# Kernel optimization log

Measured on AMD Instinct MI355X. Metric: run time of the kernel, lower is better.

## Reference

```python
import jax, jax.numpy as jnp
import numpy as np

D_MODEL = 1024
N_HEADS = 16
HEAD = D_MODEL // N_HEADS  # 64
D_FF = 4096
LN_EPS = 1e-5


def _layernorm(x, g, b):
    mu = jnp.mean(x, axis=-1, keepdims=True)
    var = jnp.mean(jnp.square(x - mu), axis=-1, keepdims=True)
    return (x - mu) * jax.lax.rsqrt(var + LN_EPS) * g + b


def _mha(q_in, k_in, v_in, Wq, Wk, Wv, bv, causal):
    # Wq/Wk/Wv: [H, d_model, head]; bv: [H, head] (value proj has bias, q/k do not)
    q = jnp.einsum('bsd,hde->bhse', q_in, Wq)
    k = jnp.einsum('btd,hde->bhte', k_in, Wk)
    v = jnp.einsum('btd,hde->bhte', v_in, Wv) + bv[None, :, None, :]
    scale = HEAD ** -0.5
    scores = jnp.einsum('bhse,bhte->bhst', q, k) * scale
    if causal:
        S, T = scores.shape[-2], scores.shape[-1]
        mask = jnp.tril(jnp.ones((S, T), dtype=bool))
        scores = jnp.where(mask, scores, -jnp.inf)
    p = jax.nn.softmax(scores, axis=-1)
    o = jnp.einsum('bhst,bhte->bhse', p, v)  # [B,H,S,head]
    B, H, S, E = o.shape
    return o.transpose(0, 2, 1, 3).reshape(B, S, H * E)  # concat heads in order


def setup_inputs() -> dict:
    key = jax.random.key(0)
    ks = jax.random.split(key, 20)
    B, S, T = 2, 2048, 2048
    sd = D_MODEL ** -0.5
    inp = {
        'input_tensor': jax.random.normal(ks[0], (B, S, D_MODEL), jnp.float32),
        'encoder_output': jax.random.normal(ks[1], (B, T, D_MODEL), jnp.float32),
        # masked self-attention params
        'Wq1': jax.random.normal(ks[2], (N_HEADS, D_MODEL, HEAD), jnp.float32) * sd,
        'Wk1': jax.random.normal(ks[3], (N_HEADS, D_MODEL, HEAD), jnp.float32) * sd,
        'Wv1': jax.random.normal(ks[4], (N_HEADS, D_MODEL, HEAD), jnp.float32) * sd,
        'bv1': jnp.zeros((N_HEADS, HEAD), jnp.float32),
        # cross-attention params
        'Wq2': jax.random.normal(ks[5], (N_HEADS, D_MODEL, HEAD), jnp.float32) * sd,
        'Wk2': jax.random.normal(ks[6], (N_HEADS, D_MODEL, HEAD), jnp.float32) * sd,
        'Wv2': jax.random.normal(ks[7], (N_HEADS, D_MODEL, HEAD), jnp.float32) * sd,
        'bv2': jnp.zeros((N_HEADS, HEAD), jnp.float32),
        # layernorms
        'g1': jnp.ones((D_MODEL,), jnp.float32), 'be1': jnp.zeros((D_MODEL,), jnp.float32),
        'g2': jnp.ones((D_MODEL,), jnp.float32), 'be2': jnp.zeros((D_MODEL,), jnp.float32),
        'g3': jnp.ones((D_MODEL,), jnp.float32), 'be3': jnp.zeros((D_MODEL,), jnp.float32),
        # FFN
        'Wf1': jax.random.normal(ks[8], (D_MODEL, D_FF), jnp.float32) * sd,
        'bf1': jnp.zeros((D_FF,), jnp.float32),
        'Wf2': jax.random.normal(ks[9], (D_FF, D_MODEL), jnp.float32) * (D_FF ** -0.5),
        'bf2': jnp.zeros((D_MODEL,), jnp.float32),
    }
    return inp


def reference(input_tensor, encoder_output, Wq1, Wk1, Wv1, bv1, Wq2, Wk2, Wv2, bv2,
              g1, be1, g2, be2, g3, be3, Wf1, bf1, Wf2, bf2):
    x = input_tensor
    # masked (causal) self-attention; dropout is identity in eval
    sa = _mha(x, x, x, Wq1, Wk1, Wv1, bv1, causal=True)
    x = _layernorm(sa + input_tensor, g1, be1)
    # cross-attention with encoder output (no mask)
    ca = _mha(x, encoder_output, encoder_output, Wq2, Wk2, Wv2, bv2, causal=False)
    x = _layernorm(x + ca, g2, be2)
    # FFN
    ffn = jax.nn.relu(x @ Wf1 + bf1) @ Wf2 + bf2
    x = _layernorm(x + ffn, g3, be3)
    return x
```

## Files before the change

kernel.cpp:

```cpp
#include <hip/hip_runtime.h>
#include <stdint.h>
#include <stddef.h>

typedef __attribute__((ext_vector_type(8))) short short8;
typedef __attribute__((ext_vector_type(4))) short short4_t;
typedef __attribute__((ext_vector_type(4))) float float4_t;
typedef __attribute__((ext_vector_type(4))) unsigned uint4_t;

#define DEV static __device__ __forceinline__

#define QSCALE 0.18033688011112042f

DEV short f2bf(float f) {
  unsigned u = __builtin_bit_cast(unsigned, f);
  u = (u + 0x7FFFu + ((u >> 16) & 1u)) >> 16;
  return (short)(unsigned short)u;
}

DEV void load_lds16(const short* g, short* l) {
  __builtin_amdgcn_global_load_lds((const __attribute__((address_space(1))) void*)g,
                                   (__attribute__((address_space(3))) void*)l,
                                   16, 0, 0);
}

__global__ __launch_bounds__(256) void transpose_cvt(const float* __restrict__ src,
                                                     short* __restrict__ dst,
                                                     int R, int C) {
  __shared__ float t[64][65];
  src += (size_t)blockIdx.z * R * C;
  dst += (size_t)blockIdx.z * R * C;
  const int tid = threadIdx.x;
  const int r0 = blockIdx.y * 64, c0 = blockIdx.x * 64;
#pragma unroll
  for (int i = 0; i < 16; i++) {
    int r = i * 4 + (tid >> 6);
    t[r][tid & 63] = src[(size_t)(r0 + r) * C + c0 + (tid & 63)];
  }
  __syncthreads();
#pragma unroll
  for (int i = 0; i < 16; i++) {
    int c = i * 4 + (tid >> 6);
    dst[(size_t)(c0 + c) * R + r0 + (tid & 63)] = f2bf(t[tid & 63][c]);
  }
}

__global__ __launch_bounds__(256) void cvt_bf16(const float* __restrict__ in,
                                                short* __restrict__ out, int n4) {
  int i = blockIdx.x * 256 + threadIdx.x;
  if (i < n4) {
    float4_t v = ((const float4_t*)in)[i];
    short4_t o;
    o.x = f2bf(v.x); o.y = f2bf(v.y); o.z = f2bf(v.z); o.w = f2bf(v.w);
    ((short4_t*)out)[i] = o;
  }
}

struct GemmArgs {
  const short* A;
  const short* Bt;
  int M, N, K;
  float* outf;
  short* outb;
  short* Qo;
  short* Ko;
  short* Vt;
  const float* bias;
};

template <int MODE>
DEV void scatter1(const GemmArgs& args, int row, int col, float v) {
  if constexpr (MODE == 0) {
    int sel = col >> 10, cc = col & 1023;
    int h = cc >> 6, e = cc & 63;
    int b_ = row >> 11, s = row & 2047;
    if (sel == 0)
      args.Qo[(((size_t)(b_ * 16 + h)) * 2048 + s) * 64 + e] = f2bf(v * QSCALE);
    else if (sel == 1)
      args.Ko[(((size_t)(b_ * 16 + h)) * 2048 + s) * 64 + e] = f2bf(v);
    else {
      v += args.bias[cc];
      args.Vt[(((size_t)(b_ * 16 + h)) * 64 + e) * 2048 + s] = f2bf(v);
    }
  } else if constexpr (MODE == 1) {
    int h = col >> 6, e = col & 63;
    int b_ = row >> 11, s = row & 2047;
    args.Qo[(((size_t)(b_ * 16 + h)) * 2048 + s) * 64 + e] = f2bf(v * QSCALE);
  } else if constexpr (MODE == 2) {
    int sel = col >> 10, cc = col & 1023;
    int h = cc >> 6, e = cc & 63;
    int b_ = row >> 11, s = row & 2047;
    if (sel == 0)
      args.Ko[(((size_t)(b_ * 16 + h)) * 2048 + s) * 64 + e] = f2bf(v);
    else {
      v += args.bias[cc];
      args.Vt[(((size_t)(b_ * 16 + h)) * 64 + e) * 2048 + s] = f2bf(v);
    }
  } else if constexpr (MODE == 3) {
    v += args.bias[col];
    v = v > 0.f ? v : 0.f;
    args.outb[(size_t)row * args.N + col] = f2bf(v);
  } else {
    v += args.bias[col];
    args.outf[(size_t)row * args.N + col] = v;
  }
}

template <int MODE>
__global__ __launch_bounds__(256) void gemm_k(GemmArgs args) {
  constexpr int BM = 128, BK = 64;
  __shared__ short As[2][BM * BK];
  __shared__ short Bs[2][BM * BK];
  const int tid = threadIdx.x;
  const int lane = tid & 63;
  const int w = tid >> 6;
  const int wr = w >> 1, wc = w & 1;

  const int nwgx = gridDim.x;
  const int nwg = nwgx * gridDim.y;
  const int orig = blockIdx.y * nwgx + blockIdx.x;
  const int q8 = nwg >> 3;
  const int swz = (orig & 7) * q8 + (orig >> 3);
  const int row0 = (swz / nwgx) * BM;
  const int col0 = (swz % nwgx) * BM;

  const int K = args.K;
  const short* Ab = args.A + (size_t)row0 * K;
  const short* Bb = args.Bt + (size_t)col0 * K;
  float4_t acc[4][4] = {};
  const int r = lane & 15, kg = lane >> 4, rx = r & 7;

  auto stage = [&](int buf, int k0) {
#pragma unroll
    for (int i = 0; i < 4; i++) {
      int c = i * 256 + tid;
      int rw = c >> 3, sc = (c & 7) ^ (rw & 7);
      load_lds16(Ab + (size_t)rw * K + k0 + sc * 8, &As[buf][c * 8]);
    }
#pragma unroll
    for (int i = 0; i < 4; i++) {
      int c = i * 256 + tid;
      int rw = c >> 3, sc = (c & 7) ^ (rw & 7);
      load_lds16(Bb + (size_t)rw * K + k0 + sc * 8, &Bs[buf][c * 8]);
    }
  };

  stage(0, 0);
  __syncthreads();
  int buf = 0;
  const int nk = K / BK;
  for (int t = 0; t < nk; t++) {
    if (t + 1 < nk) stage(buf ^ 1, (t + 1) * BK);
#pragma unroll
    for (int kk = 0; kk < BK; kk += 32) {
      const int ch = kk >> 3;
      short8 a[4], b[4];
#pragma unroll
      for (int m = 0; m < 4; m++)
        a[m] = *(const short8*)&As[buf][(wr * 64 + m * 16 + r) * BK + ((ch + kg) ^ rx) * 8];
#pragma unroll
      for (int n = 0; n < 4; n++)
        b[n] = *(const short8*)&Bs[buf][(wc * 64 + n * 16 + r) * BK + ((ch + kg) ^ rx) * 8];
#pragma unroll
      for (int m = 0; m < 4; m++)
#pragma unroll
        for (int n = 0; n < 4; n++)
          acc[m][n] = __builtin_amdgcn_mfma_f32_16x16x32_bf16(a[m], b[n], acc[m][n], 0, 0, 0);
    }
    __syncthreads();
    buf ^= 1;
  }

#pragma unroll
  for (int m = 0; m < 4; m++)
#pragma unroll
    for (int n = 0; n < 4; n++)
#pragma unroll
      for (int j = 0; j < 4; j++)
        scatter1<MODE>(args, row0 + wr * 64 + m * 16 + kg * 4 + j,
                       col0 + wc * 64 + n * 16 + r, acc[m][n][j]);
}

template <int MODE>
__global__ __launch_bounds__(512, 2) void gemm256_k(GemmArgs args) {
  extern __shared__ short lds[];
  const int tid = threadIdx.x;
  const int lane = tid & 63;
  const int w = tid >> 6;
  const int wr = w >> 2, wc = w & 3;

  const int nwgx = gridDim.x;
  const int nwg = nwgx * gridDim.y;
  const int orig = blockIdx.y * nwgx + blockIdx.x;
  const int q8 = nwg >> 3;
  const int swz = (orig & 7) * q8 + (orig >> 3);
  const int row0 = (swz / nwgx) * 256;
  const int col0 = (swz % nwgx) * 256;

  const int K = args.K;
  const short* Ab = args.A + (size_t)row0 * K;
  const short* Bb = args.Bt + (size_t)col0 * K;
  const int r = lane & 15, kg = lane >> 4, rx = r & 7;
  float4_t acc[8][4] = {};

  auto stage = [&](int buf, int k0) {
    short* Ad = lds + buf * 16384;
    short* Bd = lds + 32768 + buf * 16384;
#pragma unroll
    for (int i = 0; i < 4; i++) {
      int c = i * 512 + tid;
      int rw = c >> 3, sc = (c & 7) ^ (rw & 7);
      load_lds16(Ab + (size_t)rw * K + k0 + sc * 8, Ad + c * 8);
    }
#pragma unroll
    for (int i = 0; i < 4; i++) {
      int c = i * 512 + tid;
      int rw = c >> 3, sc = (c & 7) ^ (rw & 7);
      load_lds16(Bb + (size_t)rw * K + k0 + sc * 8, Bd + c * 8);
    }
  };

  stage(0, 0);
  __syncthreads();
  int buf = 0;
  const int nk = K / 64;
  for (int t = 0; t < nk; t++) {
    if (t + 1 < nk) stage(buf ^ 1, (t + 1) * 64);
    const short* Ar = lds + buf * 16384;
    const short* Br = lds + 32768 + buf * 16384;
#pragma unroll
    for (int kk = 0; kk < 64; kk += 32) {
      const int ch = kk >> 3;
      short8 a[8], b[4];
#pragma unroll
      for (int m = 0; m < 8; m++)
        a[m] = *(const short8*)&Ar[(wr * 128 + m * 16 + r) * 64 + ((ch + kg) ^ rx) * 8];
#pragma unroll
      for (int n = 0; n < 4; n++)
        b[n] = *(const short8*)&Br[(wc * 64 + n * 16 + r) * 64 + ((ch + kg) ^ rx) * 8];
#pragma unroll
      for (int m = 0; m < 8; m++)
#pragma unroll
        for (int n = 0; n < 4; n++)
          acc[m][n] = __builtin_amdgcn_mfma_f32_16x16x32_bf16(a[m], b[n], acc[m][n], 0, 0, 0);
    }
    __syncthreads();
    buf ^= 1;
  }

#pragma unroll
  for (int m = 0; m < 8; m++)
#pragma unroll
    for (int n = 0; n < 4; n++)
#pragma unroll
      for (int j = 0; j < 4; j++)
        scatter1<MODE>(args, row0 + wr * 128 + m * 16 + kg * 4 + j,
                       col0 + wc * 64 + n * 16 + r, acc[m][n][j]);
}

template <bool CAUSAL>
__global__ __launch_bounds__(256) void attn_k(const short* __restrict__ Q,
                                              const short* __restrict__ Kq,
                                              const short* __restrict__ Vt,
                                              float* __restrict__ Out) {
  __shared__ short kst[2][64 * 64];
  __shared__ short vst[2][64 * 64];
  __shared__ unsigned p_lds[4][16 * 32];
  const int tid = threadIdx.x;
  const int lane = tid & 63;
  const int w = tid >> 6;
  const int bh = blockIdx.y;
  const int b_ = bh >> 4, h = bh & 15;
  const int q0 = blockIdx.x * 64 + w * 16;
  const int r = lane & 15, kg = lane >> 4;
  const int rx = r & 7;
  const size_t base = (size_t)bh * 2048 * 64;
  const short* Qb = Q + base;
  const short* Kb = Kq + base;
  const short* Vb = Vt + base;

  short8 q[2];
#pragma unroll
  for (int half = 0; half < 2; half++)
    q[half] = *(const short8*)&Qb[(size_t)(q0 + r) * 64 + half * 32 + kg * 8];

  float4_t o[4] = {};
  float lp = 0.f;

  const int NT = CAUSAL ? blockIdx.x + 1 : 32;
  const float4_t zero4 = {0.f, 0.f, 0.f, 0.f};

  const int c0 = tid, c1 = tid + 256;
  const int row0s = c0 >> 3, cc0 = (c0 & 7) ^ (row0s & 7);
  const int row1s = c1 >> 3, cc1 = (c1 & 7) ^ (row1s & 7);

  auto stage = [&](int buf, int kt) {
    const short* ktk = Kb + (size_t)kt * 64 * 64;
    const short* ktv = Vb + (size_t)kt * 64;
    load_lds16(ktk + row0s * 64 + cc0 * 8, &kst[buf][c0 * 8]);
    load_lds16(ktk + row1s * 64 + cc1 * 8, &kst[buf][c1 * 8]);
    load_lds16(ktv + (size_t)row0s * 2048 + cc0 * 8, &vst[buf][c0 * 8]);
    load_lds16(ktv + (size_t)row1s * 2048 + cc1 * 8, &vst[buf][c1 * 8]);
  };

  stage(0, 0);
  __syncthreads();
  int buf = 0;

  for (int kt = 0; kt < NT; kt++) {
    if (kt + 1 < NT) stage(buf ^ 1, kt + 1);

    short8 kb[4][2];
#pragma unroll
    for (int grp = 0; grp < 4; grp++)
#pragma unroll
      for (int half = 0; half < 2; half++)
        kb[grp][half] = *(const short8*)&kst[buf][(grp * 16 + r) * 64 + ((half * 4 + kg) ^ rx) * 8];

    float4_t sc[4];
    __builtin_amdgcn_s_setprio(1);
#pragma unroll
    for (int grp = 0; grp < 4; grp++) {
      float4_t t0 = __builtin_amdgcn_mfma_f32_16x16x32_bf16(kb[grp][0], q[0], zero4, 0, 0, 0);
      sc[grp] = __builtin_amdgcn_mfma_f32_16x16x32_bf16(kb[grp][1], q[1], t0, 0, 0, 0);
    }
    __builtin_amdgcn_s_setprio(0);

    float s[16];
#pragma unroll
    for (int grp = 0; grp < 4; grp++)
#pragma unroll
      for (int j = 0; j < 4; j++) s[grp * 4 + j] = sc[grp][j];

    if (CAUSAL && kt == NT - 1) {
      const int qrow = q0 + r;
#pragma unroll
      for (int grp = 0; grp < 4; grp++)
#pragma unroll
        for (int j = 0; j < 4; j++)
          if (kt * 64 + grp * 16 + kg * 4 + j > qrow) s[grp * 4 + j] = -1e30f;
    }

    float p[16];
    float ps = 0.f;
#pragma unroll
    for (int i = 0; i < 16; i++) {
      p[i] = __builtin_amdgcn_exp2f(s[i]);
      ps += p[i];
    }
    lp += ps;

    unsigned* p32 = &p_lds[w][0];
#pragma unroll
    for (int grp = 0; grp < 4; grp++) {
      unsigned pk01, pk23;
      asm("v_cvt_pk_bf16_f32 %0, %1, %2" : "=v"(pk01) : "v"(p[grp * 4 + 0]), "v"(p[grp * 4 + 1]));
      asm("v_cvt_pk_bf16_f32 %0, %1, %2" : "=v"(pk23) : "v"(p[grp * 4 + 2]), "v"(p[grp * 4 + 3]));
      int idx = r * 32 + ((2 * grp + (kg >> 1)) ^ rx) * 4 + (kg & 1) * 2;
      p32[idx] = pk01;
      p32[idx + 1] = pk23;
    }
    __builtin_amdgcn_sched_barrier(0);

    short8 pa[2];
#pragma unroll
    for (int half = 0; half < 2; half++) {
      const int db = r * 32 + ((half * 4 + kg) ^ rx) * 4;
      uint4_t t;
      t.x = p32[db + 0];
      t.y = p32[db + 1];
      t.z = p32[db + 2];
      t.w = p32[db + 3];
      pa[half] = __builtin_bit_cast(short8, t);
    }

    __builtin_amdgcn_s_setprio(1);
#pragma unroll
    for (int n = 0; n < 4; n++) {
      short8 v0 = *(const short8*)&vst[buf][(n * 16 + r) * 64 + ((0 * 4 + kg) ^ rx) * 8];
      short8 v1 = *(const short8*)&vst[buf][(n * 16 + r) * 64 + ((1 * 4 + kg) ^ rx) * 8];
      o[n] = __builtin_amdgcn_mfma_f32_16x16x32_bf16(v0, pa[0], o[n], 0, 0, 0);
      o[n] = __builtin_amdgcn_mfma_f32_16x16x32_bf16(v1, pa[1], o[n], 0, 0, 0);
    }
    __builtin_amdgcn_s_setprio(0);

    __syncthreads();
    buf ^= 1;
  }

  lp += __shfl_xor(lp, 16);
  lp += __shfl_xor(lp, 32);
  const float inv = 1.0f / lp;
  float* orow = Out + ((size_t)b_ * 2048 + q0 + r) * 1024 + h * 64;
#pragma unroll
  for (int n = 0; n < 4; n++)
#pragma unroll
    for (int j = 0; j < 4; j++)
      orow[n * 16 + kg * 4 + j] = o[n][j] * inv;
}

__global__ __launch_bounds__(256) void add_ln_k(const float* __restrict__ X,
                                                const float* __restrict__ Y,
                                                const float* __restrict__ g,
                                                const float* __restrict__ be,
                                                float* __restrict__ outf,
                                                short* __restrict__ outb) {
  __shared__ float red[8];
  const int row = blockIdx.x;
  const int t = threadIdx.x;
  const int lane = t & 63, w = t >> 6;
  float4_t v = ((const float4_t*)(X + (size_t)row * 1024))[t];
  float4_t u = ((const float4_t*)(Y + (size_t)row * 1024))[t];
  v.x += u.x; v.y += u.y; v.z += u.z; v.w += u.w;
  float s = v.x + v.y + v.z + v.w;
#pragma unroll
  for (int off = 32; off >= 1; off >>= 1) s += __shfl_xor(s, off);
  if (lane == 0) red[w] = s;
  __syncthreads();
  float mean = (red[0] + red[1] + red[2] + red[3]) * (1.f / 1024.f);
  float dx = v.x - mean, dy = v.y - mean, dz = v.z - mean, dw = v.w - mean;
  float q2 = dx * dx + dy * dy + dz * dz + dw * dw;
#pragma unroll
  for (int off = 32; off >= 1; off >>= 1) q2 += __shfl_xor(q2, off);
  if (lane == 0) red[4 + w] = q2;
  __syncthreads();
  float var = (red[4] + red[5] + red[6] + red[7]) * (1.f / 1024.f);
  float rs = rsqrtf(var + 1e-5f);
  float4_t gg = ((const float4_t*)g)[t];
  float4_t bb = ((const float4_t*)be)[t];
  float4_t o;
  o.x = dx * rs * gg.x + bb.x;
  o.y = dy * rs * gg.y + bb.y;
  o.z = dz * rs * gg.z + bb.z;
  o.w = dw * rs * gg.w + bb.w;
  ((float4_t*)(outf + (size_t)row * 1024))[t] = o;
  if (outb != nullptr) {
    short4_t ob;
    ob.x = f2bf(o.x); ob.y = f2bf(o.y); ob.z = f2bf(o.z); ob.w = f2bf(o.w);
    ((short4_t*)(outb + (size_t)row * 1024))[t] = ob;
  }
}

extern "C" void kernel_launch(void* const* d_in, const int* in_sizes, int n_in,
                              void* d_out, int out_size, void* d_ws, size_t ws_size,
                              hipStream_t stream) {
  (void)in_sizes; (void)n_in; (void)out_size; (void)ws_size;
  const float* x_in = (const float*)d_in[0];
  const float* enc  = (const float*)d_in[1];
  const float* Wq1  = (const float*)d_in[2];
  const float* Wk1  = (const float*)d_in[3];
  const float* Wv1  = (const float*)d_in[4];
  const float* bv1  = (const float*)d_in[5];
  const float* Wq2  = (const float*)d_in[6];
  const float* Wk2  = (const float*)d_in[7];
  const float* Wv2  = (const float*)d_in[8];
  const float* bv2  = (const float*)d_in[9];
  const float* g1   = (const float*)d_in[10];
  const float* be1  = (const float*)d_in[11];
  const float* g2   = (const float*)d_in[12];
  const float* be2  = (const float*)d_in[13];
  const float* g3   = (const float*)d_in[14];
  const float* be3  = (const float*)d_in[15];
  const float* Wf1  = (const float*)d_in[16];
  const float* bf1  = (const float*)d_in[17];
  const float* Wf2  = (const float*)d_in[18];
  const float* bf2  = (const float*)d_in[19];
  float* out = (float*)d_out;

  (void)hipFuncSetAttribute((const void*)gemm256_k<0>,
                            hipFuncAttributeMaxDynamicSharedMemorySize, 131072);
  (void)hipFuncSetAttribute((const void*)gemm256_k<3>,
                            hipFuncAttributeMaxDynamicSharedMemorySize, 131072);

  char* ws = (char*)d_ws;
  size_t off = 0;
  auto alloc = [&](size_t bytes) -> void* {
    void* p = ws + off;
    off += (bytes + 255) & ~(size_t)255;
    return p;
  };
  short* wqkv1t = (short*)alloc((size_t)3072 * 1024 * 2);
  short* wq2t   = (short*)alloc((size_t)1024 * 1024 * 2);
  short* wkv2t  = (short*)alloc((size_t)2048 * 1024 * 2);
  short* wf1t   = (short*)alloc((size_t)4096 * 1024 * 2);
  short* wf2t   = (short*)alloc((size_t)1024 * 4096 * 2);
  short* act_bf = (short*)alloc((size_t)4096 * 1024 * 2);
  short* enc_bf = (short*)alloc((size_t)4096 * 1024 * 2);
  short* Qb     = (short*)alloc((size_t)4096 * 1024 * 2);
  short* Kb     = (short*)alloc((size_t)4096 * 1024 * 2);
  short* Vtb    = (short*)alloc((size_t)4096 * 1024 * 2);
  float* tmp_f  = (float*)alloc((size_t)4096 * 1024 * 4);
  float* xbuf   = (float*)alloc((size_t)4096 * 1024 * 4);
  short* h_bf   = (short*)alloc((size_t)4096 * 4096 * 2);

  dim3 blk(256);
  dim3 blk5(512);
  transpose_cvt<<<dim3(1, 16, 16), blk, 0, stream>>>(Wq1, wqkv1t, 1024, 64);
  transpose_cvt<<<dim3(1, 16, 16), blk, 0, stream>>>(Wk1, wqkv1t + 1024 * 1024, 1024, 64);
  transpose_cvt<<<dim3(1, 16, 16), blk, 0, stream>>>(Wv1, wqkv1t + 2 * 1024 * 1024, 1024, 64);
  transpose_cvt<<<dim3(1, 16, 16), blk, 0, stream>>>(Wq2, wq2t, 1024, 64);
  transpose_cvt<<<dim3(1, 16, 16), blk, 0, stream>>>(Wk2, wkv2t, 1024, 64);
  transpose_cvt<<<dim3(1, 16, 16), blk, 0, stream>>>(Wv2, wkv2t + 1024 * 1024, 1024, 64);
  transpose_cvt<<<dim3(64, 16, 1), blk, 0, stream>>>(Wf1, wf1t, 1024, 4096);
  transpose_cvt<<<dim3(16, 64, 1), blk, 0, stream>>>(Wf2, wf2t, 4096, 1024);
  cvt_bf16<<<4096, blk, 0, stream>>>(x_in, act_bf, 1048576);
  cvt_bf16<<<4096, blk, 0, stream>>>(enc, enc_bf, 1048576);

  GemmArgs ga;
  ga.A = act_bf; ga.Bt = wqkv1t; ga.M = 4096; ga.N = 3072; ga.K = 1024;
  ga.outf = nullptr; ga.outb = nullptr; ga.Qo = Qb; ga.Ko = Kb; ga.Vt = Vtb; ga.bias = bv1;
  gemm256_k<0><<<dim3(12, 16), blk5, 131072, stream>>>(ga);
  attn_k<true><<<dim3(32, 32), blk, 0, stream>>>(Qb, Kb, Vtb, tmp_f);
  add_ln_k<<<4096, blk, 0, stream>>>(tmp_f, x_in, g1, be1, xbuf, act_bf);

  ga.A = act_bf; ga.Bt = wq2t; ga.M = 4096; ga.N = 1024; ga.K = 1024;
  ga.Qo = Qb; ga.Ko = nullptr; ga.Vt = nullptr; ga.bias = nullptr;
  gemm_k<1><<<dim3(8, 32), blk, 0, stream>>>(ga);
  ga.A = enc_bf; ga.Bt = wkv2t; ga.M = 4096; ga.N = 2048; ga.K = 1024;
  ga.Qo = nullptr; ga.Ko = Kb; ga.Vt = Vtb; ga.bias = bv2;
  gemm_k<2><<<dim3(16, 32), blk, 0, stream>>>(ga);
  attn_k<false><<<dim3(32, 32), blk, 0, stream>>>(Qb, Kb, Vtb, tmp_f);
  add_ln_k<<<4096, blk, 0, stream>>>(xbuf, tmp_f, g2, be2, xbuf, act_bf);

  ga.A = act_bf; ga.Bt = wf1t; ga.M = 4096; ga.N = 4096; ga.K = 1024;
  ga.outb = h_bf; ga.bias = bf1; ga.Qo = nullptr; ga.Ko = nullptr; ga.Vt = nullptr;
  gemm256_k<3><<<dim3(16, 16), blk5, 131072, stream>>>(ga);
  ga.A = h_bf; ga.Bt = wf2t; ga.M = 4096; ga.N = 1024; ga.K = 4096;
  ga.outf = tmp_f; ga.outb = nullptr; ga.bias = bf2;
  gemm_k<4><<<dim3(8, 32), blk, 0, stream>>>(ga);
  add_ln_k<<<4096, blk, 0, stream>>>(xbuf, tmp_f, g3, be3, out, nullptr);
}
```

Baseline: 396.1 us.

## Split-K the FFN down-projection GEMM and fuse partial reduction into final layernorm

The second FFN GEMM (M=4096, N=1024, K=4096) now launches with a z-dimension of 2. Each slice computes half of K and writes fp32 partials into a new workspace buffer. A new add+layernorm kernel sums the residual, both partials and the bias before normalizing. The aim is to double the workgroup count (256 to 512) so the tall-K GEMM fills more compute units, at the cost of extra fp32 partial writes and reads (about 32MB).

```diff
diff --git a/kernel.cpp b/kernel.cpp
--- a/kernel.cpp
+++ b/kernel.cpp
@@ -116,14 +116,19 @@
   const int wr = w >> 1, wc = w & 1;
 
   const int nwgx = gridDim.x;
-  const int nwg = nwgx * gridDim.y;
-  const int orig = blockIdx.y * nwgx + blockIdx.x;
+  const int nxy = nwgx * gridDim.y;
+  const int nwg = nxy * gridDim.z;
+  const int orig = (blockIdx.z * gridDim.y + blockIdx.y) * nwgx + blockIdx.x;
   const int q8 = nwg >> 3;
   const int swz = (orig & 7) * q8 + (orig >> 3);
-  const int row0 = (swz / nwgx) * BM;
-  const int col0 = (swz % nwgx) * BM;
+  const int zsl = swz / nxy;
+  const int xy = swz % nxy;
+  const int row0 = (xy / nwgx) * BM;
+  const int col0 = (xy % nwgx) * BM;
 
   const int K = args.K;
+  const int kLen = K / gridDim.z;
+  const int kbase = zsl * kLen;
   const short* Ab = args.A + (size_t)row0 * K;
   const short* Bb = args.Bt + (size_t)col0 * K;
   float4_t acc[4][4] = {};
@@ -144,12 +149,12 @@
     }
   };
 
-  stage(0, 0);
+  stage(0, kbase);
   __syncthreads();
   int buf = 0;
-  const int nk = K / BK;
+  const int nk = kLen / BK;
   for (int t = 0; t < nk; t++) {
-    if (t + 1 < nk) stage(buf ^ 1, (t + 1) * BK);
+    if (t + 1 < nk) stage(buf ^ 1, kbase + (t + 1) * BK);
 #pragma unroll
     for (int kk = 0; kk < BK; kk += 32) {
       const int ch = kk >> 3;
@@ -170,14 +175,20 @@
     buf ^= 1;
   }
 
+  float* dst5 = args.outf + (size_t)zsl * args.M * args.N;
 #pragma unroll
   for (int m = 0; m < 4; m++)
 #pragma unroll
     for (int n = 0; n < 4; n++)
 #pragma unroll
-      for (int j = 0; j < 4; j++)
-        scatter1<MODE>(args, row0 + wr * 64 + m * 16 + kg * 4 + j,
-                       col0 + wc * 64 + n * 16 + r, acc[m][n][j]);
+      for (int j = 0; j < 4; j++) {
+        int row = row0 + wr * 64 + m * 16 + kg * 4 + j;
+        int col = col0 + wc * 64 + n * 16 + r;
+        if constexpr (MODE == 5)
+          dst5[(size_t)row * args.N + col] = acc[m][n][j];
+        else
+          scatter1<MODE>(args, row, col, acc[m][n][j]);
+      }
 }
 
 template <int MODE>
@@ -438,6 +449,49 @@
     ob.x = f2bf(o.x); ob.y = f2bf(o.y); ob.z = f2bf(o.z); ob.w = f2bf(o.w);
     ((short4_t*)(outb + (size_t)row * 1024))[t] = ob;
   }
+}
+
+__global__ __launch_bounds__(256) void add_ln2_k(const float* __restrict__ X,
+                                                 const float* __restrict__ P0,
+                                                 const float* __restrict__ P1,
+                                                 const float* __restrict__ bias,
+                                                 const float* __restrict__ g,
+                                                 const float* __restrict__ be,
+                                                 float* __restrict__ outf) {
+  __shared__ float red[8];
+  const int row = blockIdx.x;
+  const int t = threadIdx.x;
+  const int lane = t & 63, w = t >> 6;
+  float4_t v = ((const float4_t*)(X + (size_t)row * 1024))[t];
+  float4_t u0 = ((const float4_t*)(P0 + (size_t)row * 1024))[t];
+  float4_t u1 = ((const float4_t*)(P1 + (size_t)row * 1024))[t];
+  float4_t bi = ((const float4_t*)bias)[t];
+  v.x += u0.x + u1.x + bi.x;
+  v.y += u0.y + u1.y + bi.y;
+  v.z += u0.z + u1.z + bi.z;
+  v.w += u0.w + u1.w + bi.w;
+  float s = v.x + v.y + v.z + v.w;
+#pragma unroll
+  for (int off = 32; off >= 1; off >>= 1) s += __shfl_xor(s, off);
+  if (lane == 0) red[w] = s;
+  __syncthreads();
+  float mean = (red[0] + red[1] + red[2] + red[3]) * (1.f / 1024.f);
+  float dx = v.x - mean, dy = v.y - mean, dz = v.z - mean, dw = v.w - mean;
+  float q2 = dx * dx + dy * dy + dz * dz + dw * dw;
+#pragma unroll
+  for (int off = 32; off >= 1; off >>= 1) q2 += __shfl_xor(q2, off);
+  if (lane == 0) red[4 + w] = q2;
+  __syncthreads();
+  float var = (red[4] + red[5] + red[6] + red[7]) * (1.f / 1024.f);
+  float rs = rsqrtf(var + 1e-5f);
+  float4_t gg = ((const float4_t*)g)[t];
+  float4_t bb = ((const float4_t*)be)[t];
+  float4_t o;
+  o.x = dx * rs * gg.x + bb.x;
+  o.y = dy * rs * gg.y + bb.y;
+  o.z = dz * rs * gg.z + bb.z;
+  o.w = dw * rs * gg.w + bb.w;
+  ((float4_t*)(outf + (size_t)row * 1024))[t] = o;
 }
 
 extern "C" void kernel_launch(void* const* d_in, const int* in_sizes, int n_in,
@@ -491,6 +545,7 @@
   float* tmp_f  = (float*)alloc((size_t)4096 * 1024 * 4);
   float* xbuf   = (float*)alloc((size_t)4096 * 1024 * 4);
   short* h_bf   = (short*)alloc((size_t)4096 * 4096 * 2);
+  float* pbuf   = (float*)alloc((size_t)2 * 4096 * 1024 * 4);
 
   dim3 blk(256);
   dim3 blk5(512);
@@ -525,7 +580,8 @@
   ga.outb = h_bf; ga.bias = bf1; ga.Qo = nullptr; ga.Ko = nullptr; ga.Vt = nullptr;
   gemm256_k<3><<<dim3(16, 16), blk5, 131072, stream>>>(ga);
   ga.A = h_bf; ga.Bt = wf2t; ga.M = 4096; ga.N = 1024; ga.K = 4096;
-  ga.outf = tmp_f; ga.outb = nullptr; ga.bias = bf2;
-  gemm_k<4><<<dim3(8, 32), blk, 0, stream>>>(ga);
-  add_ln_k<<<4096, blk, 0, stream>>>(xbuf, tmp_f, g3, be3, out, nullptr);
-}
+  ga.outf = pbuf; ga.outb = nullptr; ga.bias = nullptr;
+  gemm_k<5><<<dim3(8, 32, 2), blk, 0, stream>>>(ga);
+  add_ln2_k<<<4096, blk, 0, stream>>>(xbuf, pbuf, pbuf + (size_t)4096 * 1024,
+                                      bf2, g3, be3, out);
+}
```

After: 367.7 us. -7.2%, faster.
